# Performance work log

Measured on AMD Instinct MI355X. Metric: run time of the kernel, lower is better.

## Reference

```python
import jax, jax.numpy as jnp
import numpy as np

E = 8       # num_experts
TOP_K = 2
H = 512     # hidden_size
DFF = 2048  # expert FFN inner dim (4*H)
B, S = 4, 2048


def setup_inputs() -> dict:
    key = jax.random.key(0)
    k0, k1, k2, k3 = jax.random.split(key, 4)
    return {
        "hidden_states": jax.random.normal(k0, (B, S, H), jnp.float32),
        # router gate: kaiming-ish init scaled by 0.01 (near-uniform routing)
        "gate_w": jax.random.normal(k1, (E, H), jnp.float32) * 0.01,
        "w1": jax.random.normal(k2, (E, H, DFF), jnp.float32) * (1.0 / np.sqrt(H)),
        "b1": jnp.zeros((E, DFF), jnp.float32),
        "w2": jax.random.normal(k3, (E, DFF, H), jnp.float32) * (1.0 / np.sqrt(DFF)),
        "b2": jnp.zeros((E, H), jnp.float32),
    }


def reference(hidden_states, gate_w, w1, b1, w2, b2):
    # hidden_states: (B, S, H)
    b, s, h = hidden_states.shape
    flat = hidden_states.reshape(-1, h)                 # (T, H), T = B*S

    # --- TopKRouter (eval mode: no gaussian noise) ---
    logits = flat @ gate_w.T                            # (T, E)
    top_vals, top_idx = jax.lax.top_k(logits, TOP_K)    # (T, K)
    top_w = jax.nn.softmax(top_vals, axis=-1)           # softmax over selected k only

    # combine[t, e] = routing weight of expert e for token t (0 if not selected).
    # top_k indices are distinct per token, so summing over k matches the
    # original masked scatter-add output[mask] += weight * expert_out.
    combine = jnp.sum(
        jax.nn.one_hot(top_idx, E, dtype=flat.dtype) * top_w[..., None], axis=1
    )                                                   # (T, E)

    # --- experts: dense compute per expert, weighted combine ---
    out = jnp.zeros_like(flat)
    for e in range(E):  # fixed small loop over experts (not a data dim)
        hdn = jax.nn.gelu(flat @ w1[e] + b1[e])         # (T, DFF)
        out = out + combine[:, e:e + 1] * (hdn @ w2[e] + b2[e])
    return out.reshape(b, s, h)
```

## Files before the change

kernel.cpp:

```cpp
#include <hip/hip_runtime.h>
#include <hip/hip_bf16.h>

#define E_    8
#define H_    512
#define DFF_  2048
#define T_    8192
#define NSLOT (2 * T_)

typedef float  f32x4  __attribute__((ext_vector_type(4)));
typedef short  bf16x8 __attribute__((ext_vector_type(8)));

static __device__ __forceinline__ ushort f2bf(float f) {
  union { float f; unsigned u; } v; v.f = f;
  unsigned r = v.u + 0x7FFFu + ((v.u >> 16) & 1u);
  return (ushort)(r >> 16);
}

static __device__ __forceinline__ void gload16(const void* g, void* l) {
  __builtin_amdgcn_global_load_lds((const __attribute__((address_space(1))) void*)g,
                                   (__attribute__((address_space(3))) void*)l, 16, 0, 0);
}

__global__ void route_cast_kernel(const float* __restrict__ x, const float* __restrict__ gw,
                                  ushort* __restrict__ xb,
                                  float* __restrict__ slotw, int* __restrict__ slote) {
  int tokn = (blockIdx.x * blockDim.x + threadIdx.x) >> 6;
  int lane = threadIdx.x & 63;
  if (tokn >= T_) return;
  const float4* xr = (const float4*)(x + (size_t)tokn * H_ + lane * 8);
  float4 x0 = xr[0], x1 = xr[1];
  ushort v[8] = {f2bf(x0.x), f2bf(x0.y), f2bf(x0.z), f2bf(x0.w),
                 f2bf(x1.x), f2bf(x1.y), f2bf(x1.z), f2bf(x1.w)};
  *(uint4*)(xb + (size_t)tokn * H_ + lane * 8) = *(uint4*)v;

  float acc[E_];
#pragma unroll
  for (int e = 0; e < E_; ++e) {
    const float4* gr = (const float4*)(gw + e * H_ + lane * 8);
    float4 g0 = gr[0], g1 = gr[1];
    acc[e] = x0.x*g0.x + x0.y*g0.y + x0.z*g0.z + x0.w*g0.w
           + x1.x*g1.x + x1.y*g1.y + x1.z*g1.z + x1.w*g1.w;
  }
#pragma unroll
  for (int e = 0; e < E_; ++e) {
#pragma unroll
    for (int off = 32; off; off >>= 1)
      acc[e] += __shfl_xor(acc[e], off);
  }
  if (lane == 0) {
    float v1 = -1e30f, v2 = -1e30f; int i1 = 0, i2 = 0;
#pragma unroll
    for (int e = 0; e < E_; ++e) {
      float vv = acc[e];
      if (vv > v1)      { v2 = v1; i2 = i1; v1 = vv; i1 = e; }
      else if (vv > v2) { v2 = vv; i2 = e; }
    }
    float ex = expf(v2 - v1);
    float inv = 1.0f / (1.0f + ex);
    slote[2 * tokn] = i1;     slotw[2 * tokn] = inv;
    slote[2 * tokn + 1] = i2; slotw[2 * tokn + 1] = ex * inv;
  }
}

__global__ __launch_bounds__(1024) void listbuild_kernel(
    const int* __restrict__ slote, int* __restrict__ counts, int* __restrict__ lslot) {
  int tid = threadIdx.x, lane = tid & 63, wv = tid >> 6;
  int base = tid * 16;
  int myexp[16];
  unsigned char cnt[E_] = {0, 0, 0, 0, 0, 0, 0, 0};
#pragma unroll
  for (int i = 0; i < 16; ++i) {
    int e = slote[base + i];
    myexp[i] = e;
    cnt[e]++;
  }
  unsigned long long lo = 0, hi = 0;
#pragma unroll
  for (int e = 0; e < 4; ++e) {
    lo |= (unsigned long long)cnt[e] << (16 * e);
    hi |= (unsigned long long)cnt[e + 4] << (16 * e);
  }
  unsigned long long mylo = lo, myhi = hi;
#pragma unroll
  for (int off = 1; off < 64; off <<= 1) {
    unsigned long long tl = __shfl_up(lo, off);
    unsigned long long th = __shfl_up(hi, off);
    if (lane >= off) { lo += tl; hi += th; }
  }
  __shared__ unsigned long long wtotlo[16], wtothi[16];
  __shared__ unsigned long long wbaselo[16], wbasehi[16];
  if (lane == 63) { wtotlo[wv] = lo; wtothi[wv] = hi; }
  __syncthreads();
  if (tid == 0) {
    unsigned long long rl = 0, rh = 0;
#pragma unroll
    for (int w2 = 0; w2 < 16; ++w2) {
      wbaselo[w2] = rl; wbasehi[w2] = rh;
      rl += wtotlo[w2]; rh += wtothi[w2];
    }
#pragma unroll
    for (int e = 0; e < 4; ++e) {
      counts[e]     = (int)((rl >> (16 * e)) & 0xFFFF);
      counts[e + 4] = (int)((rh >> (16 * e)) & 0xFFFF);
    }
  }
  __syncthreads();
  unsigned long long exlo = wbaselo[wv] + lo - mylo;
  unsigned long long exhi = wbasehi[wv] + hi - myhi;
  int pos[E_];
#pragma unroll
  for (int e = 0; e < 4; ++e) {
    pos[e]     = (int)((exlo >> (16 * e)) & 0xFFFF);
    pos[e + 4] = (int)((exhi >> (16 * e)) & 0xFFFF);
  }
#pragma unroll
  for (int i = 0; i < 16; ++i) {
    int e = myexp[i];
    lslot[e * T_ + pos[e]] = base + i;
    pos[e]++;
  }
}

__global__ void transpose_cast_kernel(const float* __restrict__ in,
                                      ushort* __restrict__ out, int R, int C) {
  int e = blockIdx.z, r0 = blockIdx.y * 64, c0 = blockIdx.x * 64;
  __shared__ float tile[64][65];
  int t = threadIdx.x;
  int row = t >> 2, seg = t & 3;
  const float* src = in + ((size_t)e * R + r0 + row) * C + c0 + seg * 16;
#pragma unroll
  for (int i = 0; i < 4; ++i) {
    float4 v = *(const float4*)(src + i * 4);
    tile[row][seg * 16 + i * 4 + 0] = v.x;
    tile[row][seg * 16 + i * 4 + 1] = v.y;
    tile[row][seg * 16 + i * 4 + 2] = v.z;
    tile[row][seg * 16 + i * 4 + 3] = v.w;
  }
  __syncthreads();
  int c = t >> 2;
  ushort vals[16];
#pragma unroll
  for (int j = 0; j < 16; ++j) vals[j] = f2bf(tile[seg * 16 + j][c]);
  ushort* dst = out + ((size_t)e * C + c0 + c) * R + r0 + seg * 16;
  *(uint4*)(dst)     = *(uint4*)&vals[0];
  *(uint4*)(dst + 8) = *(uint4*)&vals[8];
}

__global__ __launch_bounds__(256, 2) void gemm1_kernel(
    const ushort* __restrict__ xb, const ushort* __restrict__ w1t,
    const float* __restrict__ b1, const int* __restrict__ counts,
    const int* __restrict__ lslot, ushort* __restrict__ hdn, int c0, int DC) {
  int bid = blockIdx.x;
  int e = bid & (E_ - 1);
  int nx = DC / 128;
  int bx = (bid >> 3) % nx;
  int by = (bid >> 3) / nx;
  int cnt = counts[e];
  int m0 = by * 128;
  if (m0 >= cnt) return;
  int n0 = c0 + bx * 128;

  __shared__ ushort sA[128 * 64];
  __shared__ ushort sB[128 * 64];
  int tid = threadIdx.x, lane = tid & 63, wid = tid >> 6;
  int wm = wid >> 1, wn = wid & 1;
  const int* lst = lslot + e * T_;
  const ushort* w1e = w1t + (size_t)e * DFF_ * H_;

  int lrow = lane >> 3;
  int scol = ((lane & 7) ^ lrow) * 8;

  const ushort* asrc[4]; const ushort* bsrc[4];
#pragma unroll
  for (int is = 0; is < 4; ++is) {
    int row = (wid * 4 + is) * 8 + lrow;
    int r = m0 + row; if (r > cnt - 1) r = cnt - 1;
    asrc[is] = xb + (size_t)(lst[r] >> 1) * H_ + scol;
    bsrc[is] = w1e + (size_t)(n0 + row) * H_ + scol;
  }

  f32x4 acc[4][4];
#pragma unroll
  for (int i = 0; i < 4; ++i)
#pragma unroll
    for (int j = 0; j < 4; ++j) acc[i][j] = (f32x4){0.f, 0.f, 0.f, 0.f};

  for (int k0 = 0; k0 < H_; k0 += 64) {
    __syncthreads();
#pragma unroll
    for (int is = 0; is < 4; ++is) {
      gload16(asrc[is] + k0, &sA[(wid * 4 + is) * 512]);
      gload16(bsrc[is] + k0, &sB[(wid * 4 + is) * 512]);
    }
    __syncthreads();
#pragma unroll
    for (int s = 0; s < 2; ++s) {
      bf16x8 af[4], bfr[4];
#pragma unroll
      for (int i = 0; i < 4; ++i) {
        int row = wm * 64 + i * 16 + (lane & 15);
        af[i] = *(const bf16x8*)(&sA[row * 64 + (((s * 4 + (lane >> 4)) ^ (row & 7)) * 8)]);
      }
#pragma unroll
      for (int i = 0; i < 4; ++i) {
        int row = wn * 64 + i * 16 + (lane & 15);
        bfr[i] = *(const bf16x8*)(&sB[row * 64 + (((s * 4 + (lane >> 4)) ^ (row & 7)) * 8)]);
      }
#pragma unroll
      for (int i = 0; i < 4; ++i)
#pragma unroll
        for (int j = 0; j < 4; ++j)
          acc[i][j] = __builtin_amdgcn_mfma_f32_16x16x32_bf16(af[i], bfr[j], acc[i][j], 0, 0, 0);
    }
  }

  int cl = lane & 15, rg = lane >> 4;
  float b1v[4];
#pragma unroll
  for (int j = 0; j < 4; ++j) b1v[j] = b1[e * DFF_ + n0 + wn * 64 + j * 16 + cl];
#pragma unroll
  for (int i = 0; i < 4; ++i) {
    int rbase = m0 + wm * 64 + i * 16 + rg * 4;
#pragma unroll
    for (int r = 0; r < 4; ++r) {
      int gr = rbase + r;
      if (gr < cnt) {
        ushort* hrow = hdn + (size_t)lst[gr] * DC + (n0 - c0) + wn * 64 + cl;
#pragma unroll
        for (int j = 0; j < 4; ++j) {
          float v = acc[i][j][r] + b1v[j];
          float t2 = v + 0.044715f * v * v * v;
          float exv = __expf(1.5957691216057308f * t2);
          float th = 1.0f - 2.0f / (exv + 1.0f);
          hrow[j * 16] = f2bf(0.5f * v * (1.0f + th));
        }
      }
    }
  }
}

__global__ __launch_bounds__(256, 2) void gemm2_kernel(
    const ushort* __restrict__ hdn, const ushort* __restrict__ w2t,
    const float* __restrict__ b2, const float* __restrict__ slotw,
    const int* __restrict__ counts, const int* __restrict__ lslot,
    float* __restrict__ out, int c0, int DC, int addb) {
  int bid = blockIdx.x;
  int e = bid & (E_ - 1);
  const int nx = H_ / 128;
  int bx = (bid >> 3) % nx;
  int by = (bid >> 3) / nx;
  int cnt = counts[e];
  int m0 = by * 128;
  if (m0 >= cnt) return;
  int n0 = bx * 128;

  __shared__ ushort sA[128 * 64];
  __shared__ ushort sB[128 * 64];
  int tid = threadIdx.x, lane = tid & 63, wid = tid >> 6;
  int wm = wid >> 1, wn = wid & 1;
  const int* lst = lslot + e * T_;
  const ushort* w2e = w2t + (size_t)e * H_ * DFF_ + c0;

  int lrow = lane >> 3;
  int scol = ((lane & 7) ^ lrow) * 8;

  const ushort* asrc[4]; const ushort* bsrc[4];
#pragma unroll
  for (int is = 0; is < 4; ++is) {
    int row = (wid * 4 + is) * 8 + lrow;
    int r = m0 + row; if (r > cnt - 1) r = cnt - 1;
    asrc[is] = hdn + (size_t)lst[r] * DC + scol;
    bsrc[is] = w2e + (size_t)(n0 + row) * DFF_ + scol;
  }

  f32x4 acc[4][4];
#pragma unroll
  for (int i = 0; i < 4; ++i)
#pragma unroll
    for (int j = 0; j < 4; ++j) acc[i][j] = (f32x4){0.f, 0.f, 0.f, 0.f};

  for (int k0 = 0; k0 < DC; k0 += 64) {
    __syncthreads();
#pragma unroll
    for (int is = 0; is < 4; ++is) {
      gload16(asrc[is] + k0, &sA[(wid * 4 + is) * 512]);
      gload16(bsrc[is] + k0, &sB[(wid * 4 + is) * 512]);
    }
    __syncthreads();
#pragma unroll
    for (int s = 0; s < 2; ++s) {
      bf16x8 af[4], bfr[4];
#pragma unroll
      for (int i = 0; i < 4; ++i) {
        int row = wm * 64 + i * 16 + (lane & 15);
        af[i] = *(const bf16x8*)(&sA[row * 64 + (((s * 4 + (lane >> 4)) ^ (row & 7)) * 8)]);
      }
#pragma unroll
      for (int i = 0; i < 4; ++i) {
        int row = wn * 64 + i * 16 + (lane & 15);
        bfr[i] = *(const bf16x8*)(&sB[row * 64 + (((s * 4 + (lane >> 4)) ^ (row & 7)) * 8)]);
      }
#pragma unroll
      for (int i = 0; i < 4; ++i)
#pragma unroll
        for (int j = 0; j < 4; ++j)
          acc[i][j] = __builtin_amdgcn_mfma_f32_16x16x32_bf16(af[i], bfr[j], acc[i][j], 0, 0, 0);
    }
  }

  int cl = lane & 15, rg = lane >> 4;
  float b2v[4];
#pragma unroll
  for (int j = 0; j < 4; ++j)
    b2v[j] = addb ? b2[e * H_ + n0 + wn * 64 + j * 16 + cl] : 0.0f;
#pragma unroll
  for (int i = 0; i < 4; ++i) {
    int rbase = m0 + wm * 64 + i * 16 + rg * 4;
#pragma unroll
    for (int r = 0; r < 4; ++r) {
      int gr = rbase + r;
      if (gr < cnt) {
        int slot = lst[gr];
        float wgt = slotw[slot];
        float* orow = out + (size_t)(slot >> 1) * H_ + n0 + wn * 64 + cl;
#pragma unroll
        for (int j = 0; j < 4; ++j)
          atomicAdd(&orow[j * 16], wgt * (acc[i][j][r] + b2v[j]));
      }
    }
  }
}

extern "C" void kernel_launch(void* const* d_in, const int* in_sizes, int n_in,
                              void* d_out, int out_size, void* d_ws, size_t ws_size,
                              hipStream_t stream) {
  const float* x  = (const float*)d_in[0];
  const float* gw = (const float*)d_in[1];
  const float* w1 = (const float*)d_in[2];
  const float* b1 = (const float*)d_in[3];
  const float* w2 = (const float*)d_in[4];
  const float* b2 = (const float*)d_in[5];
  float* out = (float*)d_out;

  char* ws = (char*)d_ws;
  size_t off = 0;
  auto alloc = [&](size_t bytes) -> void* {
    void* p = ws + off; off += (bytes + 255) & ~(size_t)255; return p;
  };
  int*    counts = (int*)alloc(256);
  int*    lslot  = (int*)alloc((size_t)E_ * T_ * 4);
  float*  slotw  = (float*)alloc((size_t)NSLOT * 4);
  int*    slote  = (int*)alloc((size_t)NSLOT * 4);
  ushort* w1t    = (ushort*)alloc((size_t)E_ * DFF_ * H_ * 2);
  ushort* w2t    = (ushort*)alloc((size_t)E_ * H_ * DFF_ * 2);
  ushort* xb     = (ushort*)alloc((size_t)T_ * H_ * 2);

  int NC = 1;
  while (NC < 16 && off + (size_t)NSLOT * (DFF_ / NC) * 2 > ws_size) NC *= 2;
  int DC = DFF_ / NC;
  ushort* hdn = (ushort*)alloc((size_t)NSLOT * DC * 2);

  hipMemsetAsync(out, 0, (size_t)out_size * sizeof(float), stream);
  route_cast_kernel<<<T_ / 4, 256, 0, stream>>>(x, gw, xb, slotw, slote);
  listbuild_kernel<<<1, 1024, 0, stream>>>(slote, counts, lslot);
  transpose_cast_kernel<<<dim3(DFF_ / 64, H_ / 64, E_), 256, 0, stream>>>(w1, w1t, H_, DFF_);
  transpose_cast_kernel<<<dim3(H_ / 64, DFF_ / 64, E_), 256, 0, stream>>>(w2, w2t, DFF_, H_);

  for (int c = 0; c < NC; ++c) {
    gemm1_kernel<<<E_ * (DC / 128) * (T_ / 128), 256, 0, stream>>>(
        xb, w1t, b1, counts, lslot, hdn, c * DC, DC);
    gemm2_kernel<<<E_ * (H_ / 128) * (T_ / 128), 256, 0, stream>>>(
        hdn, w2t, b2, slotw, counts, lslot, out, c * DC, DC, c == NC - 1);
  }
}
```

Before: 171.0 us.

## Double-buffer LDS tiles in gemm2 to overlap global loads with MFMA

Gives the second expert GEMM kernel two LDS buffers for each operand and prefetches the next K-tile with direct-to-LDS loads while MFMAs run on the current tile. Synchronization changes to an explicit vmcnt wait plus s_barrier per tile. This is meant to hide global load latency behind compute. In exchange LDS use doubles to 64KB per block, which may reduce occupancy below the 2-blocks-per-SM launch bound. The loop assumes an even number of 64-wide K tiles.

```diff
diff --git a/kernel.cpp b/kernel.cpp
--- a/kernel.cpp
+++ b/kernel.cpp
@@ -254,8 +254,10 @@
   if (m0 >= cnt) return;
   int n0 = bx * 128;
 
-  __shared__ ushort sA[128 * 64];
-  __shared__ ushort sB[128 * 64];
+  __shared__ ushort sA0[128 * 64];
+  __shared__ ushort sB0[128 * 64];
+  __shared__ ushort sA1[128 * 64];
+  __shared__ ushort sB1[128 * 64];
   int tid = threadIdx.x, lane = tid & 63, wid = tid >> 6;
   int wm = wid >> 1, wn = wid & 1;
   const int* lst = lslot + e * T_;
@@ -279,34 +281,55 @@
 #pragma unroll
     for (int j = 0; j < 4; ++j) acc[i][j] = (f32x4){0.f, 0.f, 0.f, 0.f};
 
-  for (int k0 = 0; k0 < DC; k0 += 64) {
-    __syncthreads();
-#pragma unroll
-    for (int is = 0; is < 4; ++is) {
-      gload16(asrc[is] + k0, &sA[(wid * 4 + is) * 512]);
-      gload16(bsrc[is] + k0, &sB[(wid * 4 + is) * 512]);
-    }
-    __syncthreads();
-#pragma unroll
-    for (int s = 0; s < 2; ++s) {
-      bf16x8 af[4], bfr[4];
-#pragma unroll
-      for (int i = 0; i < 4; ++i) {
-        int row = wm * 64 + i * 16 + (lane & 15);
-        af[i] = *(const bf16x8*)(&sA[row * 64 + (((s * 4 + (lane >> 4)) ^ (row & 7)) * 8)]);
-      }
-#pragma unroll
-      for (int i = 0; i < 4; ++i) {
-        int row = wn * 64 + i * 16 + (lane & 15);
-        bfr[i] = *(const bf16x8*)(&sB[row * 64 + (((s * 4 + (lane >> 4)) ^ (row & 7)) * 8)]);
-      }
-#pragma unroll
-      for (int i = 0; i < 4; ++i)
-#pragma unroll
-        for (int j = 0; j < 4; ++j)
-          acc[i][j] = __builtin_amdgcn_mfma_f32_16x16x32_bf16(af[i], bfr[j], acc[i][j], 0, 0, 0);
-    }
-  }
+#define STAGE2(bufA, bufB, kk)                                              \
+  {                                                                         \
+    int k0_ = (kk) * 64;                                                    \
+    _Pragma("unroll")                                                       \
+    for (int is = 0; is < 4; ++is) {                                        \
+      gload16(asrc[is] + k0_, &bufA[(wid * 4 + is) * 512]);                 \
+      gload16(bsrc[is] + k0_, &bufB[(wid * 4 + is) * 512]);                 \
+    }                                                                       \
+  }
+
+#define COMP2(bufA, bufB)                                                   \
+  {                                                                         \
+    _Pragma("unroll")                                                       \
+    for (int s = 0; s < 2; ++s) {                                           \
+      bf16x8 af[4], bfr[4];                                                 \
+      _Pragma("unroll")                                                     \
+      for (int i = 0; i < 4; ++i) {                                         \
+        int row = wm * 64 + i * 16 + (lane & 15);                           \
+        af[i] = *(const bf16x8*)(&bufA[row * 64 + (((s * 4 + (lane >> 4)) ^ (row & 7)) * 8)]); \
+      }                                                                     \
+      _Pragma("unroll")                                                     \
+      for (int i = 0; i < 4; ++i) {                                         \
+        int row = wn * 64 + i * 16 + (lane & 15);                           \
+        bfr[i] = *(const bf16x8*)(&bufB[row * 64 + (((s * 4 + (lane >> 4)) ^ (row & 7)) * 8)]); \
+      }                                                                     \
+      _Pragma("unroll")                                                     \
+      for (int i = 0; i < 4; ++i)                                           \
+        _Pragma("unroll")                                                   \
+        for (int j = 0; j < 4; ++j)                                         \
+          acc[i][j] = __builtin_amdgcn_mfma_f32_16x16x32_bf16(af[i], bfr[j], acc[i][j], 0, 0, 0); \
+    }                                                                       \
+  }
+
+  int nt = DC / 64;
+  STAGE2(sA0, sB0, 0);
+  asm volatile("s_waitcnt vmcnt(0)" ::: "memory");
+  __builtin_amdgcn_s_barrier();
+  for (int t = 0; t < nt; t += 2) {
+    STAGE2(sA1, sB1, t + 1);
+    COMP2(sA0, sB0);
+    asm volatile("s_waitcnt vmcnt(0)" ::: "memory");
+    __builtin_amdgcn_s_barrier();
+    if (t + 2 < nt) STAGE2(sA0, sB0, t + 2);
+    COMP2(sA1, sB1);
+    asm volatile("s_waitcnt vmcnt(0)" ::: "memory");
+    __builtin_amdgcn_s_barrier();
+  }
+#undef STAGE2
+#undef COMP2
 
   int cl = lane & 15, rg = lane >> 4;
   float b2v[4];
```

Result: slower. 199.2 us (+16.5%).
